# Optimization experiments

Hardware: AMD Instinct MI355X
Metric: run time of the kernel (lower is better)

The kernel has to match this reference:

```python
import jax, jax.numpy as jnp
import numpy as np

EPS = 1e-6


def setup_inputs() -> dict:
    key = jax.random.key(0)
    k1, k2, k3, k4 = jax.random.split(key, 4)
    N, E, F = 100000, 6400000, 4
    node_features = jax.random.normal(k1, (N, F), dtype=jnp.float32)
    edge_index = jax.random.randint(k2, (2, E), 0, N, dtype=jnp.int64)
    edge_probs = jax.random.uniform(k3, (E,), dtype=jnp.float32)
    edge_params = jax.random.uniform(k4, (E, 2), dtype=jnp.float32)
    return {
        "node_features": node_features,
        "edge_index": edge_index,
        "edge_probs": edge_probs,
        "edge_params": edge_params,
    }


def reference(node_features, edge_index, edge_probs, edge_params):
    # Per-edge complex current magnitude: |(V_src - V_dst) / (R + 1e-6 + jX)|
    # (the torch code adds 1e-6 to the complex impedance, i.e. to the real part only)
    n_nodes = node_features.shape[0]
    src, dst = edge_index[0], edge_index[1]

    dv = node_features[src, :2] - node_features[dst, :2]          # [E, 2] (real, imag)
    num = jnp.sqrt(dv[:, 0] ** 2 + dv[:, 1] ** 2)                 # |V_src - V_dst|
    den = jnp.sqrt((edge_params[:, 0] + EPS) ** 2 + edge_params[:, 1] ** 2)  # |Z + eps|
    weighted_current = (num / den) * edge_probs                   # [E]

    # KCL: each node accumulates +I for incoming (node is dst), -I for outgoing (node is src)
    inflow = jax.ops.segment_sum(weighted_current, dst, num_segments=n_nodes)
    outflow = jax.ops.segment_sum(weighted_current, src, num_segments=n_nodes)
    node_sum = inflow - outflow                                   # [N]

    return jnp.mean(node_sum ** 2)
```

## Files before the change

### kernel.cpp

```cpp
#include <hip/hip_runtime.h>


#define EPS 1e-6f

#define NPASS        4
#define SCAN_BLOCKS  256
#define SCAN_THREADS 1024
#define WPB          (SCAN_THREADS / 64)
#define NWAVE        (SCAN_BLOCKS * WPB)
#define CAP          1024
#define RPP          64
#define BIN_THREADS  1024

__device__ __forceinline__ unsigned bf16b(float x)
{
    unsigned u = __float_as_uint(x);
    return (u + 0x7FFFu + ((u >> 16) & 1u)) >> 16;
}

__device__ __forceinline__ float edge_wc(const float* __restrict__ nf,
                                         int s, int d, float R, float X, float p)
{
    float2 vs = *(const float2*)(nf + ((size_t)s << 2));
    float2 vd = *(const float2*)(nf + ((size_t)d << 2));
    float dr = vs.x - vd.x;
    float di = vs.y - vd.y;
    float rr = R + EPS;
    return sqrtf(dr * dr + di * di) * rsqrtf(rr * rr + X * X) * p;
}

__global__ __launch_bounds__(SCAN_THREADS)
void kcl_scan(const float* __restrict__ nf, const int* __restrict__ ei,
              const float* __restrict__ probs, const float* __restrict__ params,
              unsigned* __restrict__ recs, int* __restrict__ counts,
              int E, int B1)
{
    const int lane = threadIdx.x & 63;
    const int wgid = blockIdx.x * WPB + (threadIdx.x >> 6);

    unsigned long long basepack = 0;

    const int stride = SCAN_BLOCKS * SCAN_THREADS * 4;
    for (int i = (blockIdx.x * SCAN_THREADS + threadIdx.x) * 4; i < E; i += stride) {
        const int m = (E - i < 4) ? (E - i) : 4;

        int4 s4 = *(const int4*)(ei + i);
        int4 d4 = *(const int4*)(ei + E + i);
        float4 pr = *(const float4*)(probs + i);
        float4 q0 = *(const float4*)(params + 2 * (size_t)i);
        float4 q1 = *(const float4*)(params + 2 * (size_t)i + 4);

        int   ss[4] = {s4.x, s4.y, s4.z, s4.w};
        int   dd[4] = {d4.x, d4.y, d4.z, d4.w};
        float pp[4] = {pr.x, pr.y, pr.z, pr.w};
        float Rk[4] = {q0.x, q0.z, q1.x, q1.z};
        float Xk[4] = {q0.y, q0.w, q1.y, q1.w};

        unsigned rec[8];
        int      bkt[8];
        #pragma unroll
        for (int e = 0; e < 4; ++e) {
            if (e < m) {
                float w = edge_wc(nf, ss[e], dd[e], Rk[e], Xk[e], pp[e]);
                int s = ss[e], d = dd[e];
                int bs = (s >= B1) + (s >= 2 * B1) + (s >= 3 * B1);
                int bd = (d >= B1) + (d >= 2 * B1) + (d >= 3 * B1);
                rec[2 * e]     = ((unsigned)(s - bs * B1) << 16) | bf16b(-w);
                bkt[2 * e]     = bs;
                rec[2 * e + 1] = ((unsigned)(d - bd * B1) << 16) | bf16b(w);
                bkt[2 * e + 1] = bd;
            } else {
                rec[2 * e] = rec[2 * e + 1] = 0;
                bkt[2 * e] = bkt[2 * e + 1] = -1;
            }
        }

        unsigned cpack = 0;
        #pragma unroll
        for (int k = 0; k < 8; ++k)
            if (bkt[k] >= 0) cpack += 1u << (bkt[k] * 8);

        unsigned long long cp64 =
              (unsigned long long)(cpack & 0xFFu)
            | ((unsigned long long)((cpack >> 8)  & 0xFFu) << 16)
            | ((unsigned long long)((cpack >> 16) & 0xFFu) << 32)
            | ((unsigned long long)((cpack >> 24) & 0xFFu) << 48);
        unsigned long long incl = cp64;
        #pragma unroll
        for (int off = 1; off < 64; off <<= 1) {
            unsigned long long t = __shfl_up(incl, (unsigned)off, 64);
            if (lane >= off) incl += t;
        }
        unsigned long long excl = incl - cp64;
        unsigned long long tot  = __shfl(incl, 63, 64);

        unsigned intra = 0;
        #pragma unroll
        for (int k = 0; k < 8; ++k) {
            int p = bkt[k];
            if (p >= 0) {
                unsigned off = (unsigned)((basepack >> (p * 16)) & 0xFFFFu)
                             + (unsigned)((excl     >> (p * 16)) & 0xFFFFu)
                             + ((intra >> (p * 8)) & 0xFFu);
                if (off < CAP)
                    recs[(size_t)(wgid * NPASS + p) * CAP + off] = rec[k];
                intra += 1u << (p * 8);
            }
        }
        basepack += tot;
    }

    if (lane < NPASS) {
        int c = (int)((basepack >> (lane * 16)) & 0xFFFFu);
        counts[wgid * NPASS + lane] = (c < CAP) ? c : CAP;
    }
}

__global__ __launch_bounds__(BIN_THREADS)
void kcl_bin(const unsigned* __restrict__ recs, const int* __restrict__ counts,
             float* __restrict__ partials, int B1)
{
    extern __shared__ float bins[];
    for (int j = threadIdx.x; j < B1; j += BIN_THREADS) bins[j] = 0.0f;
    __syncthreads();

    const int p = blockIdx.x / RPP;
    const int r = blockIdx.x % RPP;
    const int SPB = NWAVE / RPP;

    for (int t = 0; t < SPB; ++t) {
        int w   = r * SPB + t;
        int seg = w * NPASS + p;
        int cnt = counts[seg];
        const unsigned* base = recs + (size_t)seg * CAP;
        for (int j = threadIdx.x; j < cnt; j += BIN_THREADS) {
            unsigned rcd = base[j];
            atomicAdd(&bins[rcd >> 16], __uint_as_float(rcd << 16));
        }
    }
    __syncthreads();

    float* row = partials + (size_t)blockIdx.x * B1;
    for (int j = threadIdx.x; j < B1; j += BIN_THREADS) row[j] = bins[j];
}

__global__ __launch_bounds__(1024)
void kcl_reduce2(const float* __restrict__ partials, float* __restrict__ acc,
                 int N, int B1)
{
    int j = blockIdx.x * blockDim.x + threadIdx.x;
    float v = 0.0f;
    if (j < N) {
        int p   = j / B1;
        int bin = j - p * B1;
        const float* col = partials + (size_t)p * RPP * B1 + bin;
        float a0 = 0.f, a1 = 0.f, a2 = 0.f, a3 = 0.f;
        for (int rr = 0; rr < RPP; rr += 4) {
            a0 += col[(size_t)(rr + 0) * B1];
            a1 += col[(size_t)(rr + 1) * B1];
            a2 += col[(size_t)(rr + 2) * B1];
            a3 += col[(size_t)(rr + 3) * B1];
        }
        v = (a0 + a1) + (a2 + a3);
    }
    float sq = v * v;
    for (int off = 32; off > 0; off >>= 1)
        sq += __shfl_down(sq, off, 64);
    __shared__ float wsum[16];
    int lane = threadIdx.x & 63;
    int wid  = threadIdx.x >> 6;
    if (lane == 0) wsum[wid] = sq;
    __syncthreads();
    if (threadIdx.x == 0) {
        float t = 0.0f;
        int nw = blockDim.x >> 6;
        for (int w = 0; w < nw; ++w) t += wsum[w];
        atomicAdd(acc, t);
    }
}

__global__ void kcl_final(const float* __restrict__ acc, float* __restrict__ out,
                          float invN)
{
    if (blockIdx.x == 0 && threadIdx.x == 0)
        out[0] = acc[0] * invN;
}

#define A_BINS 25600
#define A_PBLK 256
#define A_PTHR 1024

__global__ __launch_bounds__(A_PTHR)
void kcl_pass(const float* __restrict__ nf, const int* __restrict__ ei,
              const float* __restrict__ probs, const float* __restrict__ params,
              const float* __restrict__ wc_in, float* __restrict__ wc_out,
              float* __restrict__ partials, int E, int lo, int cnt)
{
    extern __shared__ float bins[];
    for (int j = threadIdx.x; j < cnt; j += A_PTHR) bins[j] = 0.0f;
    __syncthreads();

    int i0     = (blockIdx.x * A_PTHR + threadIdx.x) * 4;
    int stride = gridDim.x * A_PTHR * 4;
    for (int i = i0; i < E; i += stride) {
        if (i + 4 <= E) {
            int4 s4 = *(const int4*)(ei + i);
            int4 d4 = *(const int4*)(ei + E + i);
            int ss[4] = {s4.x, s4.y, s4.z, s4.w};
            int dd[4] = {d4.x, d4.y, d4.z, d4.w};
            float w[4];
            if (wc_in) {
                float4 w4 = *(const float4*)(wc_in + i);
                w[0] = w4.x; w[1] = w4.y; w[2] = w4.z; w[3] = w4.w;
            } else {
                float4 pr = *(const float4*)(probs + i);
                float pp[4] = {pr.x, pr.y, pr.z, pr.w};
                float4 q0 = *(const float4*)(params + 2 * (size_t)i);
                float4 q1 = *(const float4*)(params + 2 * (size_t)i + 4);
                float Rk[4] = {q0.x, q0.z, q1.x, q1.z};
                float Xk[4] = {q0.y, q0.w, q1.y, q1.w};
                #pragma unroll
                for (int k = 0; k < 4; ++k)
                    w[k] = edge_wc(nf, ss[k], dd[k], Rk[k], Xk[k], pp[k]);
                if (wc_out)
                    *(float4*)(wc_out + i) = make_float4(w[0], w[1], w[2], w[3]);
            }
            #pragma unroll
            for (int k = 0; k < 4; ++k) {
                unsigned rs = (unsigned)(ss[k] - lo);
                if (rs < (unsigned)cnt) atomicAdd(&bins[rs], -w[k]);
                unsigned rd = (unsigned)(dd[k] - lo);
                if (rd < (unsigned)cnt) atomicAdd(&bins[rd],  w[k]);
            }
        } else {
            for (int t = i; t < E; ++t) {
                int s = ei[t], d = ei[E + t];
                float w;
                if (wc_in) w = wc_in[t];
                else {
                    float2 q = ((const float2*)params)[t];
                    w = edge_wc(nf, s, d, q.x, q.y, probs[t]);
                    if (wc_out) wc_out[t] = w;
                }
                unsigned rs = (unsigned)(s - lo);
                if (rs < (unsigned)cnt) atomicAdd(&bins[rs], -w);
                unsigned rd = (unsigned)(d - lo);
                if (rd < (unsigned)cnt) atomicAdd(&bins[rd],  w);
            }
        }
    }
    __syncthreads();
    float* row = partials + (size_t)blockIdx.x * A_BINS;
    for (int j = threadIdx.x; j < cnt; j += A_PTHR) row[j] = bins[j];
}

__global__ __launch_bounds__(1024)
void kcl_reduceA(const float* __restrict__ partials, float* __restrict__ acc, int cnt)
{
    int j = blockIdx.x * blockDim.x + threadIdx.x;
    float v = 0.0f;
    if (j < cnt) {
        const float* p = partials + j;
        float a0 = 0.f, a1 = 0.f, a2 = 0.f, a3 = 0.f;
        for (int b = 0; b < A_PBLK; b += 4) {
            a0 += p[(size_t)(b + 0) * A_BINS];
            a1 += p[(size_t)(b + 1) * A_BINS];
            a2 += p[(size_t)(b + 2) * A_BINS];
            a3 += p[(size_t)(b + 3) * A_BINS];
        }
        v = (a0 + a1) + (a2 + a3);
    }
    float sq = v * v;
    for (int off = 32; off > 0; off >>= 1)
        sq += __shfl_down(sq, off, 64);
    __shared__ float wsum[16];
    int lane = threadIdx.x & 63;
    int wid  = threadIdx.x >> 6;
    if (lane == 0) wsum[wid] = sq;
    __syncthreads();
    if (threadIdx.x == 0) {
        float t = 0.0f;
        int nw = blockDim.x >> 6;
        for (int w = 0; w < nw; ++w) t += wsum[w];
        atomicAdd(acc, t);
    }
}

__global__ void kcl_edge_atomic(const float* __restrict__ nf,
                                const int* __restrict__ ei,
                                const float* __restrict__ probs,
                                const float* __restrict__ params,
                                float* __restrict__ node_sum, int E)
{
    int i = blockIdx.x * blockDim.x + threadIdx.x;
    int stride = gridDim.x * blockDim.x;
    for (; i < E; i += stride) {
        int s = ei[i], d = ei[E + i];
        float2 q = ((const float2*)params)[i];
        float w = edge_wc(nf, s, d, q.x, q.y, probs[i]);
        atomicAdd(&node_sum[d],  w);
        atomicAdd(&node_sum[s], -w);
    }
}

__global__ void kcl_sos(const float* __restrict__ node_sum,
                        float* __restrict__ acc, int N)
{
    int i = blockIdx.x * blockDim.x + threadIdx.x;
    int stride = gridDim.x * blockDim.x;
    float s = 0.0f;
    for (; i < N; i += stride) { float v = node_sum[i]; s += v * v; }
    for (int off = 32; off > 0; off >>= 1)
        s += __shfl_down(s, off, 64);
    __shared__ float wsum[8];
    int lane = threadIdx.x & 63;
    int wid  = threadIdx.x >> 6;
    if (lane == 0) wsum[wid] = s;
    __syncthreads();
    if (threadIdx.x == 0) {
        float t = 0.0f;
        int nw = (blockDim.x + 63) >> 6;
        for (int w = 0; w < nw; ++w) t += wsum[w];
        atomicAdd(acc, t);
    }
}

extern "C" void kernel_launch(void* const* d_in, const int* in_sizes, int n_in,
                              void* d_out, int out_size, void* d_ws, size_t ws_size,
                              hipStream_t stream)
{
    const float* nf     = (const float*)d_in[0];
    const int*   ei     = (const int*)d_in[1];
    const float* probs  = (const float*)d_in[2];
    const float* params = (const float*)d_in[3];
    float*       out    = (float*)d_out;

    const int N = in_sizes[0] / 4;
    const int E = in_sizes[2];

    const int B1 = (N + NPASS - 1) / NPASS;
    size_t off_counts   = 256;
    size_t off_partials = off_counts + ((size_t)NWAVE * NPASS * 4 + 255) / 256 * 256;
    size_t off_recs     = off_partials +
                          ((size_t)NPASS * RPP * B1 * 4 + 255) / 256 * 256;
    size_t need_R = off_recs + (size_t)NWAVE * NPASS * CAP * 4;

    const bool okR = (ws_size >= need_R) && (E % 4 == 0) &&
                     (B1 <= 25600) && (B1 >= 1) && (N <= NPASS * B1);

    if (okR) {
        float*    acc      = (float*)d_ws;
        int*      counts   = (int*)((char*)d_ws + off_counts);
        float*    partials = (float*)((char*)d_ws + off_partials);
        unsigned* recs     = (unsigned*)((char*)d_ws + off_recs);

        hipMemsetAsync(acc, 0, sizeof(float), stream);

        kcl_scan<<<SCAN_BLOCKS, SCAN_THREADS, 0, stream>>>(
            nf, ei, probs, params, recs, counts, E, B1);

        kcl_bin<<<NPASS * RPP, BIN_THREADS, (size_t)B1 * sizeof(float), stream>>>(
            recs, counts, partials, B1);

        int rgrid = (N + 1023) / 1024;
        kcl_reduce2<<<rgrid, 1024, 0, stream>>>(partials, acc, N, B1);

        kcl_final<<<1, 64, 0, stream>>>(acc, out, 1.0f / (float)N);
        return;
    }

    const size_t a_partials = (size_t)A_PBLK * A_BINS * sizeof(float);
    const size_t need_A = 16 + a_partials;
    const size_t need_Awc = need_A + (size_t)E * sizeof(float);
    if (ws_size >= need_A) {
        float* acc      = (float*)d_ws;
        float* partials = (float*)((char*)d_ws + 16);
        float* wc       = (ws_size >= need_Awc)
                            ? (float*)((char*)d_ws + 16 + a_partials) : nullptr;
        hipMemsetAsync(acc, 0, sizeof(float), stream);
        const int npass = (N + A_BINS - 1) / A_BINS;
        for (int p = 0; p < npass; ++p) {
            int lo  = p * A_BINS;
            int cnt = (N - lo < A_BINS) ? (N - lo) : A_BINS;
            const float* wc_in  = (wc && p > 0) ? wc : nullptr;
            float*       wc_out = (wc && p == 0) ? wc : nullptr;
            kcl_pass<<<A_PBLK, A_PTHR, A_BINS * sizeof(float), stream>>>(
                nf, ei, probs, params, wc_in, wc_out, partials, E, lo, cnt);
            int rgrid = (cnt + 1023) / 1024;
            kcl_reduceA<<<rgrid, 1024, 0, stream>>>(partials, acc, cnt);
        }
        kcl_final<<<1, 64, 0, stream>>>(acc, out, 1.0f / (float)N);
        return;
    }

    {
        float* node_sum = (float*)d_ws;
        float* acc      = node_sum + N;
        hipMemsetAsync(d_ws, 0, (size_t)(N + 1) * sizeof(float), stream);
        int grid = (E + 255) / 256; if (grid > 4096) grid = 4096;
        kcl_edge_atomic<<<grid, 256, 0, stream>>>(nf, ei, probs, params, node_sum, E);
        int rgrid = (N + 255) / 256; if (rgrid > 256) rgrid = 256;
        kcl_sos<<<rgrid, 256, 0, stream>>>(node_sum, acc, N);
        kcl_final<<<1, 64, 0, stream>>>(acc, out, 1.0f / (float)N);
    }
}
```

Baseline: 184.5 us.

## Stage binned records in per-wave LDS rings and flush coalesced to global

The scan kernel now gives each wave a contiguous range of edges instead of a grid-strided one. It computes in-bucket offsets with four ballots plus popcount in place of a 64-bit packed shuffle scan. Records go into a per-wave, per-bucket LDS ring buffer and are written to global memory in full 64-lane coalesced chunks, with a drain at the end. The launch shape changes to 768 blocks of 512 threads with a smaller per-segment capacity. This targets scattered global stores and shuffle-scan overhead, at the cost of more ballots, flush loops and LDS traffic per record.

```diff
diff --git a/kernel.cpp b/kernel.cpp
--- a/kernel.cpp
+++ b/kernel.cpp
@@ -3,14 +3,16 @@
 
 #define EPS 1e-6f
 
-#define NPASS        4
-#define SCAN_BLOCKS  256
-#define SCAN_THREADS 1024
-#define WPB          (SCAN_THREADS / 64)
-#define NWAVE        (SCAN_BLOCKS * WPB)
-#define CAP          1024
-#define RPP          64
-#define BIN_THREADS  1024
+#define NPASS       4
+#define S_BLOCKS    768
+#define S_THREADS   512
+#define S_WPB       (S_THREADS / 64)
+#define NWAVE       (S_BLOCKS * S_WPB)
+#define CAP         640
+#define RING        128
+#define RPP         64
+#define BIN_THREADS 1024
+#define B1MAX       25600
 
 __device__ __forceinline__ unsigned bf16b(float x)
 {
@@ -29,38 +31,61 @@
     return sqrtf(dr * dr + di * di) * rsqrtf(rr * rr + X * X) * p;
 }
 
-__global__ __launch_bounds__(SCAN_THREADS)
-void kcl_scan(const float* __restrict__ nf, const int* __restrict__ ei,
-              const float* __restrict__ probs, const float* __restrict__ params,
-              unsigned* __restrict__ recs, int* __restrict__ counts,
-              int E, int B1)
-{
+#define FLUSH1(B, F, SLOT, SEG) \
+    while ((B) - (F) >= 64u) { \
+        unsigned idx_ = (F) + (unsigned)lane; \
+        unsigned v_ = rbase[(SLOT) * RING + (idx_ & (RING - 1))]; \
+        if (idx_ < (unsigned)CAP) (SEG)[idx_] = v_; \
+        (F) += 64u; \
+    }
+
+#define DRAIN1(B, F, SLOT, SEG) \
+    { unsigned rem_ = (B) - (F); unsigned idx_ = (F) + (unsigned)lane; \
+      if ((unsigned)lane < rem_ && idx_ < (unsigned)CAP) \
+          (SEG)[idx_] = rbase[(SLOT) * RING + (idx_ & (RING - 1))]; }
+
+__global__ __launch_bounds__(S_THREADS)
+void kcl_scan2(const float* __restrict__ nf, const int* __restrict__ ei,
+               const float* __restrict__ probs, const float* __restrict__ params,
+               unsigned* __restrict__ recs, int* __restrict__ counts,
+               int E, int B1, int EPW)
+{
+    __shared__ unsigned ring[S_WPB * NPASS * RING];
     const int lane = threadIdx.x & 63;
-    const int wgid = blockIdx.x * WPB + (threadIdx.x >> 6);
-
-    unsigned long long basepack = 0;
-
-    const int stride = SCAN_BLOCKS * SCAN_THREADS * 4;
-    for (int i = (blockIdx.x * SCAN_THREADS + threadIdx.x) * 4; i < E; i += stride) {
-        const int m = (E - i < 4) ? (E - i) : 4;
-
-        int4 s4 = *(const int4*)(ei + i);
-        int4 d4 = *(const int4*)(ei + E + i);
-        float4 pr = *(const float4*)(probs + i);
-        float4 q0 = *(const float4*)(params + 2 * (size_t)i);
-        float4 q1 = *(const float4*)(params + 2 * (size_t)i + 4);
-
-        int   ss[4] = {s4.x, s4.y, s4.z, s4.w};
-        int   dd[4] = {d4.x, d4.y, d4.z, d4.w};
-        float pp[4] = {pr.x, pr.y, pr.z, pr.w};
-        float Rk[4] = {q0.x, q0.z, q1.x, q1.z};
-        float Xk[4] = {q0.y, q0.w, q1.y, q1.w};
-
+    const int wv   = threadIdx.x >> 6;
+    const int wgid = blockIdx.x * S_WPB + wv;
+    unsigned* rbase = ring + wv * (NPASS * RING);
+
+    unsigned base0 = 0, base1 = 0, base2 = 0, base3 = 0;
+    unsigned fl0 = 0, fl1 = 0, fl2 = 0, fl3 = 0;
+    unsigned* seg0 = recs + (size_t)(wgid * NPASS + 0) * CAP;
+    unsigned* seg1 = recs + (size_t)(wgid * NPASS + 1) * CAP;
+    unsigned* seg2 = recs + (size_t)(wgid * NPASS + 2) * CAP;
+    unsigned* seg3 = recs + (size_t)(wgid * NPASS + 3) * CAP;
+
+    const unsigned long long lt = (1ull << lane) - 1ull;
+
+    int start = wgid * EPW;
+    int end   = start + EPW; if (end > E) end = E;
+
+    for (int wb = start; wb < end; wb += 256) {
+        int i = wb + lane * 4;
+        bool valid = (i + 4 <= end);
         unsigned rec[8];
         int      bkt[8];
-        #pragma unroll
-        for (int e = 0; e < 4; ++e) {
-            if (e < m) {
+        if (valid) {
+            int4 s4 = *(const int4*)(ei + i);
+            int4 d4 = *(const int4*)(ei + E + i);
+            float4 pr = *(const float4*)(probs + i);
+            float4 q0 = *(const float4*)(params + 2 * (size_t)i);
+            float4 q1 = *(const float4*)(params + 2 * (size_t)i + 4);
+            int   ss[4] = {s4.x, s4.y, s4.z, s4.w};
+            int   dd[4] = {d4.x, d4.y, d4.z, d4.w};
+            float pp[4] = {pr.x, pr.y, pr.z, pr.w};
+            float Rk[4] = {q0.x, q0.z, q1.x, q1.z};
+            float Xk[4] = {q0.y, q0.w, q1.y, q1.w};
+            #pragma unroll
+            for (int e = 0; e < 4; ++e) {
                 float w = edge_wc(nf, ss[e], dd[e], Rk[e], Xk[e], pp[e]);
                 int s = ss[e], d = dd[e];
                 int bs = (s >= B1) + (s >= 2 * B1) + (s >= 3 * B1);
@@ -69,50 +94,48 @@
                 bkt[2 * e]     = bs;
                 rec[2 * e + 1] = ((unsigned)(d - bd * B1) << 16) | bf16b(w);
                 bkt[2 * e + 1] = bd;
-            } else {
-                rec[2 * e] = rec[2 * e + 1] = 0;
-                bkt[2 * e] = bkt[2 * e + 1] = -1;
             }
-        }
-
-        unsigned cpack = 0;
-        #pragma unroll
-        for (int k = 0; k < 8; ++k)
-            if (bkt[k] >= 0) cpack += 1u << (bkt[k] * 8);
-
-        unsigned long long cp64 =
-              (unsigned long long)(cpack & 0xFFu)
-            | ((unsigned long long)((cpack >> 8)  & 0xFFu) << 16)
-            | ((unsigned long long)((cpack >> 16) & 0xFFu) << 32)
-            | ((unsigned long long)((cpack >> 24) & 0xFFu) << 48);
-        unsigned long long incl = cp64;
-        #pragma unroll
-        for (int off = 1; off < 64; off <<= 1) {
-            unsigned long long t = __shfl_up(incl, (unsigned)off, 64);
-            if (lane >= off) incl += t;
-        }
-        unsigned long long excl = incl - cp64;
-        unsigned long long tot  = __shfl(incl, 63, 64);
-
-        unsigned intra = 0;
+        } else {
+            #pragma unroll
+            for (int k = 0; k < 8; ++k) { bkt[k] = -1; rec[k] = 0; }
+        }
+
         #pragma unroll
         for (int k = 0; k < 8; ++k) {
-            int p = bkt[k];
-            if (p >= 0) {
-                unsigned off = (unsigned)((basepack >> (p * 16)) & 0xFFFFu)
-                             + (unsigned)((excl     >> (p * 16)) & 0xFFFFu)
-                             + ((intra >> (p * 8)) & 0xFFu);
-                if (off < CAP)
-                    recs[(size_t)(wgid * NPASS + p) * CAP + off] = rec[k];
-                intra += 1u << (p * 8);
+            int b = bkt[k];
+            unsigned long long m0 = __ballot(b == 0);
+            unsigned long long m1 = __ballot(b == 1);
+            unsigned long long m2 = __ballot(b == 2);
+            unsigned long long m3 = __ballot(b == 3);
+            if (b >= 0) {
+                unsigned long long mm = (b == 0) ? m0 : (b == 1) ? m1
+                                      : (b == 2) ? m2 : m3;
+                unsigned bb = (b == 0) ? base0 : (b == 1) ? base1
+                            : (b == 2) ? base2 : base3;
+                unsigned off = bb + (unsigned)__popcll(mm & lt);
+                rbase[b * RING + (off & (RING - 1))] = rec[k];
             }
-        }
-        basepack += tot;
-    }
-
-    if (lane < NPASS) {
-        int c = (int)((basepack >> (lane * 16)) & 0xFFFFu);
-        counts[wgid * NPASS + lane] = (c < CAP) ? c : CAP;
+            base0 += (unsigned)__popcll(m0);
+            base1 += (unsigned)__popcll(m1);
+            base2 += (unsigned)__popcll(m2);
+            base3 += (unsigned)__popcll(m3);
+            FLUSH1(base0, fl0, 0, seg0)
+            FLUSH1(base1, fl1, 1, seg1)
+            FLUSH1(base2, fl2, 2, seg2)
+            FLUSH1(base3, fl3, 3, seg3)
+        }
+    }
+
+    DRAIN1(base0, fl0, 0, seg0)
+    DRAIN1(base1, fl1, 1, seg1)
+    DRAIN1(base2, fl2, 2, seg2)
+    DRAIN1(base3, fl3, 3, seg3)
+
+    if (lane == 0) {
+        counts[wgid * NPASS + 0] = (int)(base0 < CAP ? base0 : CAP);
+        counts[wgid * NPASS + 1] = (int)(base1 < CAP ? base1 : CAP);
+        counts[wgid * NPASS + 2] = (int)(base2 < CAP ? base2 : CAP);
+        counts[wgid * NPASS + 3] = (int)(base3 < CAP ? base3 : CAP);
     }
 }
 
@@ -124,13 +147,12 @@
     for (int j = threadIdx.x; j < B1; j += BIN_THREADS) bins[j] = 0.0f;
     __syncthreads();
 
-    const int p = blockIdx.x / RPP;
-    const int r = blockIdx.x % RPP;
+    const int p   = blockIdx.x / RPP;
+    const int r   = blockIdx.x % RPP;
     const int SPB = NWAVE / RPP;
 
     for (int t = 0; t < SPB; ++t) {
-        int w   = r * SPB + t;
-        int seg = w * NPASS + p;
+        int seg = (r * SPB + t) * NPASS + p;
         int cnt = counts[seg];
         const unsigned* base = recs + (size_t)seg * CAP;
         for (int j = threadIdx.x; j < cnt; j += BIN_THREADS) {
@@ -338,17 +360,18 @@
     const int N = in_sizes[0] / 4;
     const int E = in_sizes[2];
 
-    const int B1 = (N + NPASS - 1) / NPASS;
+    const int B1  = (N + NPASS - 1) / NPASS;
+    const int EPW = (((E + NWAVE - 1) / NWAVE + 3) / 4) * 4;
     size_t off_counts   = 256;
     size_t off_partials = off_counts + ((size_t)NWAVE * NPASS * 4 + 255) / 256 * 256;
     size_t off_recs     = off_partials +
                           ((size_t)NPASS * RPP * B1 * 4 + 255) / 256 * 256;
-    size_t need_R = off_recs + (size_t)NWAVE * NPASS * CAP * 4;
-
-    const bool okR = (ws_size >= need_R) && (E % 4 == 0) &&
-                     (B1 <= 25600) && (B1 >= 1) && (N <= NPASS * B1);
-
-    if (okR) {
+    size_t need_S = off_recs + (size_t)NWAVE * NPASS * CAP * 4;
+
+    const bool okS = (ws_size >= need_S) && (E % 4 == 0) && (E > 0) &&
+                     (B1 <= B1MAX) && (B1 >= 1) && (N <= NPASS * B1);
+
+    if (okS) {
         float*    acc      = (float*)d_ws;
         int*      counts   = (int*)((char*)d_ws + off_counts);
         float*    partials = (float*)((char*)d_ws + off_partials);
@@ -356,8 +379,8 @@
 
         hipMemsetAsync(acc, 0, sizeof(float), stream);
 
-        kcl_scan<<<SCAN_BLOCKS, SCAN_THREADS, 0, stream>>>(
-            nf, ei, probs, params, recs, counts, E, B1);
+        kcl_scan2<<<S_BLOCKS, S_THREADS, 0, stream>>>(
+            nf, ei, probs, params, recs, counts, E, B1, EPW);
 
         kcl_bin<<<NPASS * RPP, BIN_THREADS, (size_t)B1 * sizeof(float), stream>>>(
             recs, counts, partials, B1);
```

Measured after the change: 156.8 us. 15.0% less time.
